# Performance work log

Hardware: AMD Instinct MI355X
Metric: run time of the kernel (lower is better)

The kernel has to match this reference:

```python
import jax, jax.numpy as jnp
import numpy as np
from jax import lax

K_SIZE = 7
STRIDES = (2, 2, 2, 3)

def causal_conv_block(x, w, b, stride):
    # x: (B, Cin, L); w: (Cout, Cin, K); left-pad K-1 for causality
    xp = jnp.pad(x, ((0, 0), (0, 0), (K_SIZE - 1, 0)))
    y = lax.conv_general_dilated(xp, w, window_strides=(stride,), padding='VALID',
                                 dimension_numbers=('NCH', 'OIH', 'NCH'))
    return jax.nn.elu(y + b[None, :, None])

def vq_indices(z, codebook):
    # z: (B, D, T); codebook: (K, D) -> indices (B, T)
    zt = jnp.transpose(z, (0, 2, 1))                      # (B, T, D)
    d = (jnp.sum(zt * zt, axis=-1, keepdims=True)
         - 2.0 * jnp.einsum('btd,kd->btk', zt, codebook)
         + jnp.sum(codebook * codebook, axis=-1)[None, None, :])  # (B, T, K)
    return jnp.argmin(d, axis=-1)

def setup_inputs() -> dict:
    key = jax.random.key(0)
    ks = jax.random.split(key, 16)
    B, L = 64, 48000
    chans = [1, 16, 32, 64, 64]  # in->out schedule from min(64, 16*2**i)
    inp = {'x': jax.random.normal(ks[0], (B, 1, L), dtype=jnp.float32)}
    for i in range(4):
        cin, cout = chans[i], chans[i + 1]
        scale = 1.0 / np.sqrt(cin * K_SIZE)
        inp[f'w{i}'] = jax.random.normal(ks[1 + 2 * i], (cout, cin, K_SIZE), jnp.float32) * scale
        inp[f'b{i}'] = jax.random.normal(ks[2 + 2 * i], (cout,), jnp.float32) * 0.01
    # pre_quant: 64 -> LATENT_DIM*NUM_CODEBOOKS = 128
    inp['wq'] = jax.random.normal(ks[10], (128, 64, K_SIZE), jnp.float32) * (1.0 / np.sqrt(64 * K_SIZE))
    inp['bq'] = jax.random.normal(ks[11], (128,), jnp.float32) * 0.01
    inp['codebooks'] = jax.random.normal(ks[12], (2, 1024, 64), jnp.float32)  # (num_cb, K, D)
    return inp

def reference(x, w0, b0, w1, b1, w2, b2, w3, b3, wq, bq, codebooks):
    h = x
    for w, b, s in ((w0, b0, STRIDES[0]), (w1, b1, STRIDES[1]),
                    (w2, b2, STRIDES[2]), (w3, b3, STRIDES[3])):
        h = causal_conv_block(h, w, b, s)
    z_e = causal_conv_block(h, wq, bq, 1)           # (B, 128, T)
    z0, z1 = jnp.split(z_e, 2, axis=1)              # chunk along channel dim
    idx0 = vq_indices(z0, codebooks[0])             # (B, T) int
    idx1 = vq_indices(z1, codebooks[1])
    return jnp.stack([idx0, idx1], axis=0)          # (num_cb, B, T)
```

## Files before the change

### kernel.cpp

```cpp
#include <hip/hip_runtime.h>
#include <hip/hip_bf16.h>
#include <cstddef>


using bf16x8 = __attribute__((ext_vector_type(8))) short;
using s16x4  = __attribute__((ext_vector_type(4))) short;
using f32x4  = __attribute__((ext_vector_type(4))) float;

static __device__ __forceinline__ short f2bf(float f) {
    __hip_bfloat16 h = __float2bfloat16(f);
    union { __hip_bfloat16 h; short s; } u; u.h = h;
    return u.s;
}
static __device__ __forceinline__ float bf2f(short s) {
    union { unsigned u; float f; } v;
    v.u = ((unsigned)(unsigned short)s) << 16;
    return v.f;
}
static __device__ __forceinline__ void split3(float v, short& s0, short& s1, short& s2) {
    s0 = f2bf(v);  float r1 = v  - bf2f(s0);
    s1 = f2bf(r1); float r2 = r1 - bf2f(s1);
    s2 = f2bf(r2);
}
static __device__ __forceinline__ float elu(float v) {
    return v > 0.0f ? v : expm1f(v);
}

__global__ __launch_bounds__(256) void conv0_kernel(
    const float* __restrict__ x, const float* __restrict__ w,
    const float* __restrict__ bias, float* __restrict__ H0)
{
    __shared__ float xs[261];
    int tb = blockIdx.x, b = blockIdx.y;
    int t0 = tb * 128;
    int tid = threadIdx.x, lane = tid & 63;
    int wv = __builtin_amdgcn_readfirstlane(tid >> 6);

    const float* xb = x + (size_t)b * 48000;
    int g0 = t0 * 2 - 6;
    for (int i = tid; i < 261; i += 256) {
        int gx = g0 + i;
        xs[i] = (gx >= 0 && gx < 48000) ? xb[gx] : 0.0f;
    }
    __syncthreads();

    int co0 = wv * 4;
    float acc[4][2];
    #pragma unroll
    for (int c = 0; c < 4; ++c) { acc[c][0] = 0.f; acc[c][1] = 0.f; }

    float xw[2][7];
    #pragma unroll
    for (int u = 0; u < 2; ++u)
        #pragma unroll
        for (int k = 0; k < 7; ++k)
            xw[u][k] = xs[(lane + 64 * u) * 2 + k];
    #pragma unroll
    for (int c = 0; c < 4; ++c) {
        const float* wp = w + (size_t)(co0 + c) * 7;
        #pragma unroll
        for (int k = 0; k < 7; ++k) {
            float wk = wp[k];
            acc[c][0] = fmaf(wk, xw[0][k], acc[c][0]);
            acc[c][1] = fmaf(wk, xw[1][k], acc[c][1]);
        }
    }

    #pragma unroll
    for (int u = 0; u < 2; ++u) {
        int t = t0 + lane + 64 * u;
        if (t < 24000) {
            float4 vv;
            vv.x = elu(acc[0][u] + bias[co0 + 0]);
            vv.y = elu(acc[1][u] + bias[co0 + 1]);
            vv.z = elu(acc[2][u] + bias[co0 + 2]);
            vv.w = elu(acc[3][u] + bias[co0 + 3]);
            *(float4*)(H0 + ((size_t)b * 12000 + (t >> 1)) * 32 + (t & 1) * 16 + co0) = vv;
        }
    }
}

template<int CIN, int COUT, int TAPS>
__global__ void wprep3_kernel(const float* __restrict__ w, short* __restrict__ frag)
{
    constexpr int KC = CIN / 32;
    int co = threadIdx.x;
    if (co >= COUT) return;
    int mt = co >> 4, nc = co & 15;
    for (int kc = 0; kc < KC; ++kc)
        for (int k = 0; k < TAPS; ++k)
            #pragma unroll
            for (int lh = 0; lh < 4; ++lh) {
                bf16x8 p0, p1, p2;
                #pragma unroll
                for (int j = 0; j < 8; ++j) {
                    int ci = kc * 32 + lh * 8 + j;
                    float f = w[(size_t)co * CIN * 7 + ci * 7 + k];
                    short a, bb, c; split3(f, a, bb, c);
                    p0[j] = a; p1[j] = bb; p2[j] = c;
                }
                size_t base = ((size_t)(mt * KC + kc) * TAPS + k) * 3;
                int off = (lh * 16 + nc) * 8;
                *(bf16x8*)(frag + (base + 0) * 512 + off) = p0;
                *(bf16x8*)(frag + (base + 1) * 512 + off) = p1;
                *(bf16x8*)(frag + (base + 2) * 512 + off) = p2;
            }
}

template<int CINH, int COUT>
__global__ void wprep3_ps_kernel(const float* __restrict__ w, short* __restrict__ frag)
{
    constexpr int CIN = 2 * CINH;
    constexpr int KC  = CIN / 32;
    int co = threadIdx.x;
    if (co >= COUT) return;
    int mt = co >> 4, nc = co & 15;
    for (int kc = 0; kc < KC; ++kc)
        for (int m = 0; m < 4; ++m)
            #pragma unroll
            for (int lh = 0; lh < 4; ++lh) {
                bf16x8 p0, p1, p2;
                #pragma unroll
                for (int j = 0; j < 8; ++j) {
                    int cp = kc * 32 + lh * 8 + j;
                    float f;
                    if (cp < CINH)  f = w[(size_t)co * CINH * 7 + cp * 7 + 2 * m];
                    else if (m < 3) f = w[(size_t)co * CINH * 7 + (cp - CINH) * 7 + 2 * m + 1];
                    else            f = 0.0f;
                    short a, bb, c; split3(f, a, bb, c);
                    p0[j] = a; p1[j] = bb; p2[j] = c;
                }
                size_t base = ((size_t)(mt * KC + kc) * 4 + m) * 3;
                int off = (lh * 16 + nc) * 8;
                *(bf16x8*)(frag + (base + 0) * 512 + off) = p0;
                *(bf16x8*)(frag + (base + 1) * 512 + off) = p1;
                *(bf16x8*)(frag + (base + 2) * 512 + off) = p2;
            }
}

template<int S, int CIN, int COUT, int NTL, int TAPS, int PAD, int OUTMODE>
__global__ __launch_bounds__(256) void conv_mfma3_kernel(
    const float* __restrict__ Hin, const short* __restrict__ wfrag,
    const float* __restrict__ bias, float* __restrict__ Hout,
    int Lin, int Lout)
{
    constexpr int KC   = CIN / 32;
    constexpr int MT   = COUT / 16;
    constexpr int NT   = NTL * 64;
    constexpr int ROWS = (NT - 1) * S + TAPS;
    constexpr int ROWB = CIN * 2;
    constexpr int NSL  = CIN / 4;
    __shared__ __align__(16) short pl0[ROWS * CIN];
    __shared__ __align__(16) short pl1[ROWS * CIN];
    __shared__ __align__(16) short pl2[ROWS * CIN];

    int nb = blockIdx.x, b = blockIdx.y;
    int t0 = nb * NT;
    int tid = threadIdx.x, lane = tid & 63, wv = tid >> 6;
    int g0 = t0 * S - PAD;

    const float* inb = Hin + (size_t)b * Lin * CIN;
    for (int e = tid; e < ROWS * NSL; e += 256) {
        int rr = e / NSL, sl = e % NSL;
        int g = g0 + rr;
        float4 v = {0.f, 0.f, 0.f, 0.f};
        if (g >= 0 && g < Lin)
            v = *(const float4*)(inb + (size_t)g * CIN + sl * 4);
        int xr = (CIN == 64) ? (rr & 7) : ((rr >> 1) & 3);
        int byte = rr * ROWB + ((((sl >> 1) ^ xr) << 4) | ((sl & 1) << 3));
        s16x4 q0, q1, q2;
        short a0, a1, a2;
        split3(v.x, a0, a1, a2); q0[0] = a0; q1[0] = a1; q2[0] = a2;
        split3(v.y, a0, a1, a2); q0[1] = a0; q1[1] = a1; q2[1] = a2;
        split3(v.z, a0, a1, a2); q0[2] = a0; q1[2] = a1; q2[2] = a2;
        split3(v.w, a0, a1, a2); q0[3] = a0; q1[3] = a1; q2[3] = a2;
        *(s16x4*)((char*)pl0 + byte) = q0;
        *(s16x4*)((char*)pl1 + byte) = q1;
        *(s16x4*)((char*)pl2 + byte) = q2;
    }
    __syncthreads();

    f32x4 acc[NTL][MT];
    #pragma unroll
    for (int n = 0; n < NTL; ++n)
        #pragma unroll
        for (int m = 0; m < MT; ++m) acc[n][m] = (f32x4){0.f, 0.f, 0.f, 0.f};

    int ncol = lane & 15, nq = lane >> 4;

    for (int k = 0; k < TAPS; ++k) {
        #pragma unroll
        for (int kc = 0; kc < KC; ++kc) {
            int colb = (kc * 32 + nq * 8) * 2;
            bf16x8 B0[NTL], B1[NTL], B2[NTL];
            #pragma unroll
            for (int ntl = 0; ntl < NTL; ++ntl) {
                int r  = S * ((wv * NTL + ntl) * 16 + ncol) + k;
                int xr = (CIN == 64) ? (r & 7) : ((r >> 1) & 3);
                int byte = r * ROWB + (colb ^ (xr << 4));
                B0[ntl] = *(const bf16x8*)((char*)pl0 + byte);
                B1[ntl] = *(const bf16x8*)((char*)pl1 + byte);
                B2[ntl] = *(const bf16x8*)((char*)pl2 + byte);
            }
            #pragma unroll
            for (int m = 0; m < MT; ++m) {
                size_t base = ((size_t)(m * KC + kc) * TAPS + k) * 3;
                bf16x8 a0 = *(const bf16x8*)(wfrag + (base + 0) * 512 + lane * 8);
                bf16x8 a1 = *(const bf16x8*)(wfrag + (base + 1) * 512 + lane * 8);
                bf16x8 a2 = *(const bf16x8*)(wfrag + (base + 2) * 512 + lane * 8);
                #pragma unroll
                for (int ntl = 0; ntl < NTL; ++ntl) {
                    f32x4 a = acc[ntl][m];
                    a = __builtin_amdgcn_mfma_f32_16x16x32_bf16(a0, B0[ntl], a, 0, 0, 0);
                    a = __builtin_amdgcn_mfma_f32_16x16x32_bf16(a1, B0[ntl], a, 0, 0, 0);
                    a = __builtin_amdgcn_mfma_f32_16x16x32_bf16(a2, B0[ntl], a, 0, 0, 0);
                    a = __builtin_amdgcn_mfma_f32_16x16x32_bf16(a0, B1[ntl], a, 0, 0, 0);
                    a = __builtin_amdgcn_mfma_f32_16x16x32_bf16(a1, B1[ntl], a, 0, 0, 0);
                    a = __builtin_amdgcn_mfma_f32_16x16x32_bf16(a0, B2[ntl], a, 0, 0, 0);
                    acc[ntl][m] = a;
                }
            }
        }
    }

    #pragma unroll
    for (int ntl = 0; ntl < NTL; ++ntl) {
        int n = t0 + (wv * NTL + ntl) * 16 + ncol;
        if (n < Lout) {
            #pragma unroll
            for (int m = 0; m < MT; ++m) {
                int co0 = m * 16 + nq * 4;
                float4 bb = *(const float4*)(bias + co0);
                float4 vv;
                vv.x = elu(acc[ntl][m][0] + bb.x);
                vv.y = elu(acc[ntl][m][1] + bb.y);
                vv.z = elu(acc[ntl][m][2] + bb.z);
                vv.w = elu(acc[ntl][m][3] + bb.w);
                if constexpr (OUTMODE == 0) {
                    *(float4*)(Hout + ((size_t)b * Lout + n) * COUT + co0) = vv;
                } else if constexpr (OUTMODE == 1) {
                    *(float4*)(Hout + ((size_t)b * (Lout >> 1) + (n >> 1)) * (2 * COUT)
                               + (n & 1) * COUT + co0) = vv;
                } else {
                    Hout[((size_t)b * COUT + co0 + 0) * Lout + n] = vv.x;
                    Hout[((size_t)b * COUT + co0 + 1) * Lout + n] = vv.y;
                    Hout[((size_t)b * COUT + co0 + 2) * Lout + n] = vv.z;
                    Hout[((size_t)b * COUT + co0 + 3) * Lout + n] = vv.w;
                }
            }
        }
    }
}

__global__ __launch_bounds__(256) void vq_prep_kernel(
    const float* __restrict__ cbs, float* __restrict__ cc, short* __restrict__ cbf)
{
    int c = blockIdx.x * 256 + threadIdx.x;
    if (c >= 2048) return;
    int cb = c >> 10, nl = c & 1023;
    const float* row = cbs + (size_t)c * 64;
    float v[64];
    float s = 0.f;
    #pragma unroll
    for (int i = 0; i < 16; ++i) {
        float4 q = ((const float4*)row)[i];
        v[4*i+0] = q.x; v[4*i+1] = q.y; v[4*i+2] = q.z; v[4*i+3] = q.w;
        s += q.x*q.x + q.y*q.y + q.z*q.z + q.w*q.w;
    }
    cc[c] = s;
    int nt = nl >> 4, nc = nl & 15;
    #pragma unroll
    for (int kc = 0; kc < 2; ++kc)
        #pragma unroll
        for (int lh = 0; lh < 4; ++lh) {
            bf16x8 ph, pl;
            #pragma unroll
            for (int j = 0; j < 8; ++j) {
                float f = -2.0f * v[kc*32 + lh*8 + j];
                short h = f2bf(f);
                ph[j] = h;
                pl[j] = f2bf(f - bf2f(h));
            }
            size_t base = ((((size_t)cb*64 + nt)*2 + kc)*2);
            *(bf16x8*)(cbf + ((base + 0)*64 + (lh*16 + nc)) * 8) = ph;
            *(bf16x8*)(cbf + ((base + 1)*64 + (lh*16 + nc)) * 8) = pl;
        }
}

__global__ void zero_cnt_kernel(int* cnt) {
    if (threadIdx.x == 0 && blockIdx.x == 0) { cnt[0] = 0; cnt[1] = 0; }
}

#define VQ_MARGIN 0.04f

__global__ __launch_bounds__(256)
__attribute__((amdgpu_waves_per_eu(4, 4)))
void vq_mfma_kernel(
    const float* __restrict__ z, const short* __restrict__ cbf,
    const float* __restrict__ ccg, int* __restrict__ out,
    int* __restrict__ cnt, int* __restrict__ list0, int* __restrict__ list1)
{
    __shared__ __align__(16) short sbuf[16384];
    short* zf0 = sbuf;
    short* zf1 = sbuf + 8192;

    const int T = 2000;
    int mblk = blockIdx.x;
    int cb   = blockIdx.y;
    int b    = blockIdx.z;
    int t0   = mblk * 128;
    int tid  = threadIdx.x;
    int lane = tid & 63;
    int wv   = tid >> 6;
    int* list = cb ? list1 : list0;

    const float* zb = z + ((size_t)b*128 + (size_t)cb*64) * T;
    for (int e = tid; e < 128 * 8; e += 256) {
        int tl = e & 127;
        int d0 = (e >> 7) * 8;
        int tt = t0 + tl; if (tt > T - 1) tt = T - 1;
        bf16x8 hi, lo;
        #pragma unroll
        for (int jj = 0; jj < 8; ++jj) {
            float v = zb[(size_t)(d0 + jj) * T + tt];
            short h = f2bf(v);
            hi[jj] = h;
            lo[jj] = f2bf(v - bf2f(h));
        }
        int mt = tl >> 4, kc = d0 >> 5;
        int lw = ((d0 & 31) >> 3) * 16 + (tl & 15);
        int idx = ((mt*2 + kc)*64 + lw) * 8;
        *(bf16x8*)&zf0[idx] = hi;
        *(bf16x8*)&zf1[idx] = lo;
    }
    __syncthreads();

    bf16x8 ah[2][2], al[2][2];
    #pragma unroll
    for (int mtl = 0; mtl < 2; ++mtl)
        #pragma unroll
        for (int kc = 0; kc < 2; ++kc) {
            int idx = ((((wv*2+mtl)*2 + kc)*64) + lane)*8;
            ah[mtl][kc] = *(const bf16x8*)&zf0[idx];
            al[mtl][kc] = *(const bf16x8*)&zf1[idx];
        }
    __syncthreads();

    float best[2][4], second[2][4]; int bidx[2][4];
    #pragma unroll
    for (int m = 0; m < 2; ++m)
        #pragma unroll
        for (int j = 0; j < 4; ++j) { best[m][j] = 3.4e38f; second[m][j] = 3.4e38f; bidx[m][j] = 0; }

    const short* cbase = cbf + (size_t)cb * (64*2*2*64*8);
    const float* ccb   = ccg + cb * 1024;
    int c15 = lane & 15;

    {
        const float4* src = (const float4*)cbase;
        float4* dst = (float4*)sbuf;
        #pragma unroll
        for (int i = 0; i < 4; ++i) dst[tid + 256*i] = src[tid + 256*i];
    }
    __syncthreads();

    for (int ch = 0; ch < 16; ++ch) {
        short* cur = sbuf + (ch & 1) * 8192;
        short* nxt = sbuf + ((ch + 1) & 1) * 8192;
        float4 pre0, pre1, pre2, pre3;
        if (ch < 15) {
            const float4* src = (const float4*)(cbase + (size_t)(ch + 1) * 8192);
            pre0 = src[tid];       pre1 = src[tid + 256];
            pre2 = src[tid + 512]; pre3 = src[tid + 768];
        }

        #pragma unroll
        for (int ntl = 0; ntl < 4; ++ntl) {
            bf16x8 b0h = *(const bf16x8*)&cur[(((ntl*2 + 0)*2 + 0)*64 + lane)*8];
            bf16x8 b0l = *(const bf16x8*)&cur[(((ntl*2 + 0)*2 + 1)*64 + lane)*8];
            bf16x8 b1h = *(const bf16x8*)&cur[(((ntl*2 + 1)*2 + 0)*64 + lane)*8];
            bf16x8 b1l = *(const bf16x8*)&cur[(((ntl*2 + 1)*2 + 1)*64 + lane)*8];
            int  code = ch*64 + ntl*16 + c15;
            float ccv = ccb[code];
            #pragma unroll
            for (int mtl = 0; mtl < 2; ++mtl) {
                f32x4 p = {ccv, ccv, ccv, ccv};
                __builtin_amdgcn_s_setprio(1);
                p = __builtin_amdgcn_mfma_f32_16x16x32_bf16(ah[mtl][0], b0h, p, 0, 0, 0);
                p = __builtin_amdgcn_mfma_f32_16x16x32_bf16(al[mtl][0], b0h, p, 0, 0, 0);
                p = __builtin_amdgcn_mfma_f32_16x16x32_bf16(ah[mtl][0], b0l, p, 0, 0, 0);
                p = __builtin_amdgcn_mfma_f32_16x16x32_bf16(ah[mtl][1], b1h, p, 0, 0, 0);
                p = __builtin_amdgcn_mfma_f32_16x16x32_bf16(al[mtl][1], b1h, p, 0, 0, 0);
                p = __builtin_amdgcn_mfma_f32_16x16x32_bf16(ah[mtl][1], b1l, p, 0, 0, 0);
                __builtin_amdgcn_s_setprio(0);
                #pragma unroll
                for (int j = 0; j < 4; ++j) {
                    float s = p[j];
                    bool lt = s < best[mtl][j];
                    second[mtl][j] = __builtin_amdgcn_fmed3f(best[mtl][j], s, second[mtl][j]);
                    best[mtl][j]   = fminf(best[mtl][j], s);
                    bidx[mtl][j]   = lt ? code : bidx[mtl][j];
                }
            }
        }

        if (ch < 15) {
            float4* dst = (float4*)nxt;
            dst[tid]       = pre0;  dst[tid + 256] = pre1;
            dst[tid + 512] = pre2;  dst[tid + 768] = pre3;
        }
        __syncthreads();
    }

    #pragma unroll
    for (int m = 0; m < 2; ++m)
        #pragma unroll
        for (int j = 0; j < 4; ++j) {
            float bv = best[m][j], sv = second[m][j]; int bi = bidx[m][j];
            #pragma unroll
            for (int d = 1; d < 16; d <<= 1) {
                float ob = __shfl_xor(bv, d, 64);
                float os = __shfl_xor(sv, d, 64);
                int   oi = __shfl_xor(bi, d, 64);
                float loser = fmaxf(bv, ob);
                sv = fminf(fminf(sv, os), loser);
                bool sw = ob < bv;
                bv = fminf(bv, ob);
                bi = sw ? oi : bi;
            }
            if ((lane & 15) == 0) {
                int t = t0 + (wv*2 + m)*16 + (lane >> 4)*4 + j;
                if (t < T) {
                    out[((size_t)cb*64 + b)*T + t] = bi;
                    if (sv - bv < VQ_MARGIN) {
                        int pos = atomicAdd(&cnt[cb], 1);
                        list[pos] = (b << 11) | t;
                    }
                }
            }
        }
}

__global__ __launch_bounds__(256) void vq_rescore_kernel(
    const float* __restrict__ H3, const float* __restrict__ wq,
    const float* __restrict__ bq, const float* __restrict__ cbs,
    const float* __restrict__ ccg, const int* __restrict__ cnt,
    const int* __restrict__ list0, const int* __restrict__ list1,
    int* __restrict__ out)
{
    const int T = 2000;
    __shared__ float hp[4][4][448];
    __shared__ float zsh[4][4][64];
    int tid = threadIdx.x, lane = tid & 63, wv = tid >> 6;
    int cb = blockIdx.y;
    const int* list = cb ? list1 : list0;
    int count = cnt[cb];
    int gw = blockIdx.x * 4 + wv, nw = gridDim.x * 4;

    const float* cbase = cbs + (size_t)cb * 1024 * 64;
    const float* ccb   = ccg + cb * 1024;
    int d = cb * 64 + lane;
    const float4* wp = (const float4*)(wq + (size_t)d * 448);
    float bqd = bq[d];

    for (int i0 = gw * 4; i0 < count; i0 += nw * 4) {
        int bf_[4], tf_[4];
        #pragma unroll
        for (int f = 0; f < 4; ++f) {
            int idx = i0 + f; if (idx > count - 1) idx = count - 1;
            int e = list[idx];
            bf_[f] = e >> 11; tf_[f] = e & 2047;
        }

        #pragma unroll
        for (int f = 0; f < 4; ++f) {
            size_t base = (size_t)bf_[f] * T * 64;
            #pragma unroll
            for (int kk = 0; kk < 7; ++kk) {
                int a = tf_[f] - 6 + kk;
                hp[wv][f][lane * 7 + kk] = (a >= 0) ? H3[base + (size_t)a * 64 + lane] : 0.0f;
            }
        }

        float pa[4][4];
        #pragma unroll
        for (int f = 0; f < 4; ++f)
            #pragma unroll
            for (int j = 0; j < 4; ++j) pa[f][j] = 0.f;
        #pragma unroll 4
        for (int q = 0; q < 112; ++q) {
            float4 w4 = wp[q];
            #pragma unroll
            for (int f = 0; f < 4; ++f) {
                float4 h = *(const float4*)&hp[wv][f][4 * q];
                pa[f][0] = fmaf(w4.x, h.x, pa[f][0]);
                pa[f][1] = fmaf(w4.y, h.y, pa[f][1]);
                pa[f][2] = fmaf(w4.z, h.z, pa[f][2]);
                pa[f][3] = fmaf(w4.w, h.w, pa[f][3]);
            }
        }
        #pragma unroll
        for (int f = 0; f < 4; ++f) {
            float zv = (pa[f][0] + pa[f][1]) + (pa[f][2] + pa[f][3]) + bqd;
            zsh[wv][f][lane] = zv > 0.f ? zv : expm1f(zv);
        }

        float bv[4]; int bi[4];
        #pragma unroll
        for (int f = 0; f < 4; ++f) { bv[f] = 3.4e38f; bi[f] = 0; }
        for (int ii = 0; ii < 16; ++ii) {
            int code = ii * 64 + lane;
            const float4* cp = (const float4*)(cbase + (size_t)code * 64);
            float dd[4][4];
            #pragma unroll
            for (int f = 0; f < 4; ++f)
                #pragma unroll
                for (int j = 0; j < 4; ++j) dd[f][j] = 0.f;
            #pragma unroll
            for (int q = 0; q < 16; ++q) {
                float4 cv = cp[q];
                #pragma unroll
                for (int f = 0; f < 4; ++f) {
                    float4 za = *(const float4*)&zsh[wv][f][4 * q];
                    dd[f][0] = fmaf(za.x, cv.x, dd[f][0]);
                    dd[f][1] = fmaf(za.y, cv.y, dd[f][1]);
                    dd[f][2] = fmaf(za.z, cv.z, dd[f][2]);
                    dd[f][3] = fmaf(za.w, cv.w, dd[f][3]);
                }
            }
            float cc0 = ccb[code];
            #pragma unroll
            for (int f = 0; f < 4; ++f) {
                float s = fmaf(-2.0f, (dd[f][0] + dd[f][1]) + (dd[f][2] + dd[f][3]), cc0);
                if (s < bv[f]) { bv[f] = s; bi[f] = code; }
            }
        }
        #pragma unroll
        for (int ddp = 1; ddp < 64; ddp <<= 1) {
            #pragma unroll
            for (int f = 0; f < 4; ++f) {
                float ov = __shfl_xor(bv[f], ddp, 64);
                int   oi = __shfl_xor(bi[f], ddp, 64);
                if (ov < bv[f] || (ov == bv[f] && oi < bi[f])) { bv[f] = ov; bi[f] = oi; }
            }
        }
        if (lane == 0) {
            #pragma unroll
            for (int f = 0; f < 4; ++f)
                out[((size_t)cb * 64 + bf_[f]) * T + tf_[f]] = bi[f];
        }
    }
}

extern "C" void kernel_launch(void* const* d_in, const int* in_sizes, int n_in,
                              void* d_out, int out_size, void* d_ws, size_t ws_size,
                              hipStream_t stream)
{
    const float* x   = (const float*)d_in[0];
    const float* w0  = (const float*)d_in[1];
    const float* b0  = (const float*)d_in[2];
    const float* w1  = (const float*)d_in[3];
    const float* b1  = (const float*)d_in[4];
    const float* w2  = (const float*)d_in[5];
    const float* b2  = (const float*)d_in[6];
    const float* w3  = (const float*)d_in[7];
    const float* b3  = (const float*)d_in[8];
    const float* wq  = (const float*)d_in[9];
    const float* bq  = (const float*)d_in[10];
    const float* cbs = (const float*)d_in[11];
    int* out = (int*)d_out;

    char* r1 = (char*)d_ws;
    char* r2 = r1 + 98304000;
    float* H0 = (float*)r1;
    float* H1 = (float*)r2;
    float* H2 = (float*)r1;
    float* H3 = (float*)r2;
    float* z  = (float*)(r2 + 32768000);

    short* wf1 = (short*)d_out;
    short* wf2 = wf1 + 12288;
    short* wf3 = wf1 + 61440;
    short* wf4 = wf1 + 147456;

    short* cbf   = (short*)r1;
    float* cc    = (float*)(r1 + 524288);
    int*   cnt   = (int*)(r1 + 540000);
    int*   list0 = (int*)(r1 + 1000000);
    int*   list1 = (int*)(r1 + 2100000);

    wprep3_ps_kernel<16, 32><<<1, 32, 0, stream>>>(w1, wf1);
    wprep3_ps_kernel<32, 64><<<1, 64, 0, stream>>>(w2, wf2);
    wprep3_kernel<64, 64, 7><<<1, 64, 0, stream>>>(w3, wf3);
    wprep3_kernel<64, 128, 7><<<1, 128, 0, stream>>>(wq, wf4);

    conv0_kernel<<<dim3(188, 64), 256, 0, stream>>>(x, w0, b0, H0);
    conv_mfma3_kernel<1, 32, 32, 2, 4, 3, 1><<<dim3(94, 64), 256, 0, stream>>>(
        H0, wf1, b1, H1, 12000, 12000);
    conv_mfma3_kernel<1, 64, 64, 2, 4, 3, 0><<<dim3(47, 64), 256, 0, stream>>>(
        H1, wf2, b2, H2, 6000, 6000);
    conv_mfma3_kernel<3, 64, 64, 1, 7, 6, 0><<<dim3(32, 64), 256, 0, stream>>>(
        H2, wf3, b3, H3, 6000, 2000);

    vq_prep_kernel<<<8, 256, 0, stream>>>(cbs, cc, cbf);
    zero_cnt_kernel<<<1, 64, 0, stream>>>(cnt);

    conv_mfma3_kernel<1, 64, 128, 2, 7, 6, 2><<<dim3(16, 64), 256, 0, stream>>>(
        H3, wf4, bq, z, 2000, 2000);

    vq_mfma_kernel<<<dim3(16, 2, 64), 256, 0, stream>>>(z, cbf, cc, out, cnt, list0, list1);
    vq_rescore_kernel<<<dim3(512, 2), 256, 0, stream>>>(H3, wq, bq, cbs, cc, cnt, list0, list1, out);
}
```

Baseline: 644.8 us.

## Fuse first conv layer into second conv's MFMA kernel, computing layer-0 activations in LDS

Merges conv0 (scalar FMA, Cin=1) into the layer-1 MFMA convolution kernel. Each block loads the raw input window, computes the layer-0 ELU outputs for its halo rows directly into the three bf16-split LDS planes, then runs the existing 3-pass bf16 MFMA scheme. This removes the large H0 intermediate write and read through global memory and one kernel launch. The cost is recomputing halo rows per block and the scalar conv running inside the MFMA kernel's prologue.

```diff
diff --git a/kernel.cpp b/kernel.cpp
--- a/kernel.cpp
+++ b/kernel.cpp
@@ -26,56 +26,122 @@
     return v > 0.0f ? v : expm1f(v);
 }
 
-__global__ __launch_bounds__(256) void conv0_kernel(
-    const float* __restrict__ x, const float* __restrict__ w,
-    const float* __restrict__ bias, float* __restrict__ H0)
-{
-    __shared__ float xs[261];
-    int tb = blockIdx.x, b = blockIdx.y;
-    int t0 = tb * 128;
-    int tid = threadIdx.x, lane = tid & 63;
-    int wv = __builtin_amdgcn_readfirstlane(tid >> 6);
+__global__ __launch_bounds__(256) void conv01_kernel(
+    const float* __restrict__ x, const float* __restrict__ w0,
+    const float* __restrict__ b0, const short* __restrict__ wfrag,
+    const float* __restrict__ bias, float* __restrict__ Hout)
+{
+    constexpr int CIN = 32, COUT = 32, NTL = 2, TAPS = 4, S = 1;
+    constexpr int KC = 1, MT = 2, NT = 128, ROWS = 131, ROWB = 64;
+    constexpr int Lin = 12000, Lout = 12000;
+    __shared__ __align__(16) short pl0[ROWS * CIN];
+    __shared__ __align__(16) short pl1[ROWS * CIN];
+    __shared__ __align__(16) short pl2[ROWS * CIN];
+    __shared__ float xs[536];
+
+    int nb = blockIdx.x, b = blockIdx.y;
+    int t0 = nb * NT;
+    int tid = threadIdx.x, lane = tid & 63, wv = tid >> 6;
+    int g0 = t0 - 3;
 
     const float* xb = x + (size_t)b * 48000;
-    int g0 = t0 * 2 - 6;
-    for (int i = tid; i < 261; i += 256) {
-        int gx = g0 + i;
-        xs[i] = (gx >= 0 && gx < 48000) ? xb[gx] : 0.0f;
+    int xbase = 4 * g0 - 6;
+    for (int i = tid; i < 529; i += 256) {
+        int g = xbase + i;
+        xs[i] = (g >= 0 && g < 48000) ? xb[g] : 0.0f;
     }
     __syncthreads();
 
-    int co0 = wv * 4;
-    float acc[4][2];
-    #pragma unroll
-    for (int c = 0; c < 4; ++c) { acc[c][0] = 0.f; acc[c][1] = 0.f; }
-
-    float xw[2][7];
-    #pragma unroll
-    for (int u = 0; u < 2; ++u)
-        #pragma unroll
-        for (int k = 0; k < 7; ++k)
-            xw[u][k] = xs[(lane + 64 * u) * 2 + k];
-    #pragma unroll
-    for (int c = 0; c < 4; ++c) {
-        const float* wp = w + (size_t)(co0 + c) * 7;
-        #pragma unroll
-        for (int k = 0; k < 7; ++k) {
-            float wk = wp[k];
-            acc[c][0] = fmaf(wk, xw[0][k], acc[c][0]);
-            acc[c][1] = fmaf(wk, xw[1][k], acc[c][1]);
-        }
-    }
-
-    #pragma unroll
-    for (int u = 0; u < 2; ++u) {
-        int t = t0 + lane + 64 * u;
-        if (t < 24000) {
-            float4 vv;
-            vv.x = elu(acc[0][u] + bias[co0 + 0]);
-            vv.y = elu(acc[1][u] + bias[co0 + 1]);
-            vv.z = elu(acc[2][u] + bias[co0 + 2]);
-            vv.w = elu(acc[3][u] + bias[co0 + 3]);
-            *(float4*)(H0 + ((size_t)b * 12000 + (t >> 1)) * 32 + (t & 1) * 16 + co0) = vv;
+    for (int e = tid; e < ROWS * 8; e += 256) {
+        int rr = e >> 3, sl = e & 7;
+        int g = g0 + rr;
+        int ph = sl >> 2;
+        int xr = (rr >> 1) & 3;
+        int byte = rr * ROWB + ((((sl >> 1) ^ xr) << 4) | ((sl & 1) << 3));
+        bool ok = (g >= 0 && g < Lin);
+        int bx = 4 * rr + 2 * ph;
+        s16x4 q0, q1, q2;
+        #pragma unroll
+        for (int j = 0; j < 4; ++j) {
+            float v = 0.0f;
+            if (ok) {
+                int co = (sl & 3) * 4 + j;
+                const float* wp = w0 + co * 7;
+                float acc = 0.f;
+                #pragma unroll
+                for (int k = 0; k < 7; ++k)
+                    acc = fmaf(wp[k], xs[bx + k], acc);
+                v = elu(acc + b0[co]);
+            }
+            short a0, a1, a2;
+            split3(v, a0, a1, a2);
+            q0[j] = a0; q1[j] = a1; q2[j] = a2;
+        }
+        *(s16x4*)((char*)pl0 + byte) = q0;
+        *(s16x4*)((char*)pl1 + byte) = q1;
+        *(s16x4*)((char*)pl2 + byte) = q2;
+    }
+    __syncthreads();
+
+    f32x4 acc[NTL][MT];
+    #pragma unroll
+    for (int n = 0; n < NTL; ++n)
+        #pragma unroll
+        for (int m = 0; m < MT; ++m) acc[n][m] = (f32x4){0.f, 0.f, 0.f, 0.f};
+
+    int ncol = lane & 15, nq = lane >> 4;
+
+    for (int k = 0; k < TAPS; ++k) {
+        #pragma unroll
+        for (int kc = 0; kc < KC; ++kc) {
+            int colb = (kc * 32 + nq * 8) * 2;
+            bf16x8 B0[NTL], B1[NTL], B2[NTL];
+            #pragma unroll
+            for (int ntl = 0; ntl < NTL; ++ntl) {
+                int r  = S * ((wv * NTL + ntl) * 16 + ncol) + k;
+                int xr = (r >> 1) & 3;
+                int byte = r * ROWB + (colb ^ (xr << 4));
+                B0[ntl] = *(const bf16x8*)((char*)pl0 + byte);
+                B1[ntl] = *(const bf16x8*)((char*)pl1 + byte);
+                B2[ntl] = *(const bf16x8*)((char*)pl2 + byte);
+            }
+            #pragma unroll
+            for (int m = 0; m < MT; ++m) {
+                size_t base = ((size_t)(m * KC + kc) * TAPS + k) * 3;
+                bf16x8 a0 = *(const bf16x8*)(wfrag + (base + 0) * 512 + lane * 8);
+                bf16x8 a1 = *(const bf16x8*)(wfrag + (base + 1) * 512 + lane * 8);
+                bf16x8 a2 = *(const bf16x8*)(wfrag + (base + 2) * 512 + lane * 8);
+                #pragma unroll
+                for (int ntl = 0; ntl < NTL; ++ntl) {
+                    f32x4 a = acc[ntl][m];
+                    a = __builtin_amdgcn_mfma_f32_16x16x32_bf16(a0, B0[ntl], a, 0, 0, 0);
+                    a = __builtin_amdgcn_mfma_f32_16x16x32_bf16(a1, B0[ntl], a, 0, 0, 0);
+                    a = __builtin_amdgcn_mfma_f32_16x16x32_bf16(a2, B0[ntl], a, 0, 0, 0);
+                    a = __builtin_amdgcn_mfma_f32_16x16x32_bf16(a0, B1[ntl], a, 0, 0, 0);
+                    a = __builtin_amdgcn_mfma_f32_16x16x32_bf16(a1, B1[ntl], a, 0, 0, 0);
+                    a = __builtin_amdgcn_mfma_f32_16x16x32_bf16(a0, B2[ntl], a, 0, 0, 0);
+                    acc[ntl][m] = a;
+                }
+            }
+        }
+    }
+
+    #pragma unroll
+    for (int ntl = 0; ntl < NTL; ++ntl) {
+        int n = t0 + (wv * NTL + ntl) * 16 + ncol;
+        if (n < Lout) {
+            #pragma unroll
+            for (int m = 0; m < MT; ++m) {
+                int co0 = m * 16 + nq * 4;
+                float4 bb = *(const float4*)(bias + co0);
+                float4 vv;
+                vv.x = elu(acc[ntl][m][0] + bb.x);
+                vv.y = elu(acc[ntl][m][1] + bb.y);
+                vv.z = elu(acc[ntl][m][2] + bb.z);
+                vv.w = elu(acc[ntl][m][3] + bb.w);
+                *(float4*)(Hout + ((size_t)b * (Lout >> 1) + (n >> 1)) * (2 * COUT)
+                           + (n & 1) * COUT + co0) = vv;
+            }
         }
     }
 }
@@ -572,7 +638,6 @@
 
     char* r1 = (char*)d_ws;
     char* r2 = r1 + 98304000;
-    float* H0 = (float*)r1;
     float* H1 = (float*)r2;
     float* H2 = (float*)r1;
     float* H3 = (float*)r2;
@@ -594,9 +659,7 @@
     wprep3_kernel<64, 64, 7><<<1, 64, 0, stream>>>(w3, wf3);
     wprep3_kernel<64, 128, 7><<<1, 128, 0, stream>>>(wq, wf4);
 
-    conv0_kernel<<<dim3(188, 64), 256, 0, stream>>>(x, w0, b0, H0);
-    conv_mfma3_kernel<1, 32, 32, 2, 4, 3, 1><<<dim3(94, 64), 256, 0, stream>>>(
-        H0, wf1, b1, H1, 12000, 12000);
+    conv01_kernel<<<dim3(94, 64), 256, 0, stream>>>(x, w0, b0, wf1, b1, H1);
     conv_mfma3_kernel<1, 64, 64, 2, 4, 3, 0><<<dim3(47, 64), 256, 0, stream>>>(
         H1, wf2, b2, H2, 6000, 6000);
     conv_mfma3_kernel<3, 64, 64, 1, 7, 6, 0><<<dim3(32, 64), 256, 0, stream>>>(
```

New measurement: 637.1 us (median of 2 runs). Within noise of the previous version (-1.2%).
